# Optimization experiments

Hardware: AMD Instinct MI355X
Metric: run time of the kernel (lower is better)

The kernel has to match this reference:

```python
import jax, jax.numpy as jnp
from jax import lax
import numpy as np

B, N_VARS, M_CLAUSES, K_DIM = 1024, 64, 256, 12
MAX_ITER = 12


def setup_inputs() -> dict:
    key = jax.random.key(0)
    k1, k2, k3, k4 = jax.random.split(key, 4)
    z = jax.random.uniform(k1, (B, N_VARS), dtype=jnp.float32)          # input probabilities
    S = jax.random.normal(k2, (M_CLAUSES, N_VARS + 1), dtype=jnp.float32) * 0.2  # learnable clause matrix (col 0 = truth var)
    w = jax.random.uniform(k3, (M_CLAUSES,), dtype=jnp.float32)          # learnable clause weights
    r = jax.random.normal(k4, (B, N_VARS, K_DIM), dtype=jnp.float32)     # random init directions
    return {"z": z, "S": S, "w": w, "r": r, "max_iter": MAX_ITER}


def _mixing(z, S, w, r, max_iter):
    Bsz, n = z.shape
    m, N = S.shape  # N = n + 1 (truth variable is column 0)
    k = r.shape[-1]
    eps = jnp.float32(1e-8)

    # truth direction v_T = e_0
    vT = jnp.zeros((k,), dtype=z.dtype).at[0].set(1.0)

    # random unit directions orthogonal to v_T (zero out component along e_0)
    r_perp = r.at[..., 0].set(0.0)
    r_perp = r_perp / jnp.maximum(jnp.linalg.norm(r_perp, axis=-1, keepdims=True), eps)

    # SATNet init: v_i = -cos(pi z_i) v_T + sin(pi z_i) r_perp_i
    ang = jnp.pi * z
    Vvars = -jnp.cos(ang)[..., None] * vT + jnp.sin(ang)[..., None] * r_perp  # [B,n,k]
    V = jnp.concatenate([jnp.broadcast_to(vT, (Bsz, 1, k)), Vvars], axis=1)   # [B,N,k]

    Sw = S * w[:, None]                       # weighted clause matrix [m,N]
    W = jnp.einsum('mn,bnk->bmk', Sw, V)      # running product Sw @ V, [B,m,k]
    snrm = jnp.sum(Sw * Sw, axis=0)           # ||s_i||^2 per variable, [N]

    def coord_step(carry, i):
        V, W = carry
        s_i = Sw[:, i]                         # [m]
        v_old = V[:, i, :]                     # [B,k]
        g = jnp.einsum('bmk,m->bk', W, s_i) - snrm[i] * v_old
        v_new = -g / jnp.maximum(jnp.linalg.norm(g, axis=-1, keepdims=True), eps)
        W = W + (v_new - v_old)[:, None, :] * s_i[None, :, None]  # rank-1 update
        V = V.at[:, i, :].set(v_new)
        return (V, W), None

    def sweep(carry, _):
        carry, _ = lax.scan(coord_step, carry, jnp.arange(1, N))  # coordinate descent over variables
        return carry, None

    (V, _), _ = lax.scan(sweep, (V, W), None, length=max_iter)

    # output probabilities: z_i = arccos(-v_i . v_T) / pi
    cos = jnp.clip(-V[:, 1:, 0], -1.0 + 1e-6, 1.0 - 1e-6)
    return jnp.arccos(cos) / jnp.pi


def reference(z, S, w, r, max_iter):
    return _mixing(z, S, w, r, max_iter)
```

## Files before the change

kernel.cpp:

```cpp
#include <hip/hip_runtime.h>
#include <math.h>

#define BATCH 1024
#define NV    64
#define MC    256
#define KD    12
#define PI_F  3.14159265358979323846f

#define CBUF   4544
#define C0OFF  4352
#define DGAOFF 4416
#define DGBOFF 4480

typedef float f2 __attribute__((ext_vector_type(2)));

template <int CTRL>
__device__ __forceinline__ float dpp_addf(float x) {
  int y = __builtin_amdgcn_update_dpp(0, __float_as_int(x), CTRL, 0xF, 0xF, true);
  return x + __int_as_float(y);
}
__device__ __forceinline__ float allreduce16(float x) {
  x = dpp_addf<0xB1>(x);
  x = dpp_addf<0x4E>(x);
  x = dpp_addf<0x124>(x);
  x = dpp_addf<0x128>(x);
  return x;
}
__device__ __forceinline__ float readlane63(float x) {
  return __int_as_float(__builtin_amdgcn_readlane(__float_as_int(x), 63));
}

__global__ void compute_C_kernel(const float* __restrict__ S,
                                 const float* __restrict__ w,
                                 float* __restrict__ Cg, int nsplit) {
  const int q = blockIdx.x;
  const int mc = blockIdx.y;
  const int j = threadIdx.x;
  if (j > NV) return;
  const int v = (q + 1) % 64 + 1;
  const int mlen = MC / nsplit;
  const int m0 = mc * mlen;
  float a0 = 0.f, a1 = 0.f, a2 = 0.f, a3 = 0.f;
  for (int m = m0; m < m0 + mlen; m += 4) {
    const float w0 = w[m], w1 = w[m + 1], w2 = w[m + 2], w3 = w[m + 3];
    a0 = fmaf(S[(m + 0) * (NV + 1) + v] * w0 * w0, S[(m + 0) * (NV + 1) + j], a0);
    a1 = fmaf(S[(m + 1) * (NV + 1) + v] * w1 * w1, S[(m + 1) * (NV + 1) + j], a1);
    a2 = fmaf(S[(m + 2) * (NV + 1) + v] * w2 * w2, S[(m + 2) * (NV + 1) + j], a2);
    a3 = fmaf(S[(m + 3) * (NV + 1) + v] * w3 * w3, S[(m + 3) * (NV + 1) + j], a3);
  }
  const float acc = (a0 + a1) + (a2 + a3);
  float* buf = Cg + mc * CBUF;
  const int p1 = (v == 1) ? 64 : (v - 1);
  const int p2 = (v == 1) ? 63 : (v == 2) ? 64 : (v - 2);
  if (j == 0) buf[C0OFF + q] = acc;
  if (j == p1) buf[DGAOFF + (v - 1)] = acc;
  if (j == p2) buf[DGBOFF + (v - 1)] = acc;
  if (j > 0) {
    const float st = (j == v || j == p1 || j == p2) ? 0.f : acc;
    buf[q * 68 + (j - 1)] = st;
  }
}

__global__ __launch_bounds__(256, 1) void mixing_kernel(
    const float* __restrict__ z, const float* __restrict__ r,
    const float* __restrict__ Cg, const int* __restrict__ max_iter_p,
    float* __restrict__ out, int nsplit) {
  __shared__ float Ls[CBUF];

  const int t = threadIdx.x;
  const int l = t & 63;
  const int kq = l >> 4;
  const int n16 = l & 15;
  const int b = blockIdx.x * 4 + (t >> 6);
  const int max_iter = max_iter_p[0];

  {
    const float4* src = (const float4*)Cg;
    float4* dst = (float4*)Ls;
    for (int idx = t; idx < CBUF / 4; idx += 256) {
      float4 a = src[idx];
      for (int u = 1; u < nsplit; ++u) {
        const float4 p = src[u * (CBUF / 4) + idx];
        a.x += p.x; a.y += p.y; a.z += p.z; a.w += p.w;
      }
      dst[idx] = a;
    }
  }

  const float row0 = (kq == 0) ? 1.f : 0.f;

  f2 V01[4];
  float V2[4];
  #pragma unroll
  for (int s = 0; s < 4; ++s) {
    const int n = 4 * n16 + s;
    const float zv = z[b * NV + n];
    float rp[3];
    float ssp = 0.f;
    #pragma unroll
    for (int j = 0; j < 3; ++j) {
      const int k = 3 * kq + j;
      rp[j] = (k == 0) ? 0.f : r[(b * NV + n) * KD + k];
      ssp = fmaf(rp[j], rp[j], ssp);
    }
    ssp += __shfl_xor(ssp, 16, 64);
    ssp += __shfl_xor(ssp, 32, 64);
    const float inv = 1.f / fmaxf(sqrtf(ssp), 1e-8f);
    float sn, cs;
    sincosf(PI_F * zv, &sn, &cs);
    float vv[3];
    #pragma unroll
    for (int j = 0; j < 3; ++j) {
      const int k = 3 * kq + j;
      vv[j] = (k == 0) ? -cs : sn * rp[j] * inv;
    }
    V01[s].x = vv[0];
    V01[s].y = vv[1];
    V2[s] = vv[2];
  }

  __syncthreads();

  const float4* C4   = (const float4*)Ls;
  const float4* C04  = (const float4*)(Ls + C0OFF);
  const float4* DgA4 = (const float4*)(Ls + DGAOFF);
  const float4* DgB4 = (const float4*)(Ls + DGBOFF);

  f2 P01, vp1_01, vp2_01;
  float P2, vp1_2, vp2_2;

  {
    const float4 ce = C4[63 * 17 + n16];
    const float c0 = Ls[C0OFF + 63];
    f2 q01 = ce.x * V01[0];
    float q2 = ce.x * V2[0];
    q01 = __builtin_elementwise_fma((f2){ce.y, ce.y}, V01[1], q01);
    q2 = fmaf(ce.y, V2[1], q2);
    q01 = __builtin_elementwise_fma((f2){ce.z, ce.z}, V01[2], q01);
    q2 = fmaf(ce.z, V2[2], q2);
    q01 = __builtin_elementwise_fma((f2){ce.w, ce.w}, V01[3], q01);
    q2 = fmaf(ce.w, V2[3], q2);
    q01.x = allreduce16(q01.x);
    q01.y = allreduce16(q01.y);
    q2 = allreduce16(q2);
    q01.x = fmaf(row0, c0, q01.x);
    P01 = q01; P2 = q2;
    const int src = l | 15;
    vp1_01.x = __shfl(V01[3].x, src, 64);
    vp1_01.y = __shfl(V01[3].y, src, 64);
    vp1_2    = __shfl(V2[3],    src, 64);
    vp2_01.x = __shfl(V01[2].x, src, 64);
    vp2_01.y = __shfl(V01[2].y, src, 64);
    vp2_2    = __shfl(V2[2],    src, 64);
  }

  float4 cbA[4], cbB[4], c0A, c0B, daA, daB, dbA, dbB;

  auto prefetch = [&](float4 cb[4], float4& c0b, float4& dab, float4& dbb, int g) {
    #pragma unroll
    for (int s = 0; s < 4; ++s) cb[s] = C4[(4 * g + s) * 17 + n16];
    c0b = C04[g];
    dab = DgA4[g];
    dbb = DgB4[g];
  };

  auto do_group = [&](int ii, const float4 cb[4], const float4& c0b,
                      const float4& dab, const float4& dbb) {
    const bool own  = (n16 == ii);
    const bool ownP = (n16 == ((ii + 15) & 15));
    const float* c0p = &c0b.x;
    const float* dap = &dab.x;
    const float* dbp = &dbb.x;
    #pragma unroll
    for (int s = 0; s < 4; ++s) {
      const float4 ce = cb[s];
      const float db = dbp[s], da = dap[s];

      f2 g01 = __builtin_elementwise_fma((f2){db, db}, vp2_01, P01);
      float g2 = fmaf(db, vp2_2, P2);
      g01 = __builtin_elementwise_fma((f2){da, da}, vp1_01, g01);
      g2 = fmaf(da, vp1_2, g2);

      f2 q01 = ce.x * V01[0];
      float q2 = ce.x * V2[0];
      q01 = __builtin_elementwise_fma((f2){ce.y, ce.y}, V01[1], q01);
      q2 = fmaf(ce.y, V2[1], q2);
      q01 = __builtin_elementwise_fma((f2){ce.z, ce.z}, V01[2], q01);
      q2 = fmaf(ce.z, V2[2], q2);
      q01 = __builtin_elementwise_fma((f2){ce.w, ce.w}, V01[3], q01);
      q2 = fmaf(ce.w, V2[3], q2);

      float n2p = g01.x * g01.x;
      n2p = fmaf(g01.y, g01.y, n2p);
      n2p = fmaf(g2, g2, n2p);

      n2p = dpp_addf<0x142>(n2p);
      q01.x = dpp_addf<0xB1>(q01.x);
      q01.y = dpp_addf<0xB1>(q01.y);
      q2 = dpp_addf<0xB1>(q2);
      n2p = dpp_addf<0x143>(n2p);
      q01.x = dpp_addf<0x4E>(q01.x);
      q01.y = dpp_addf<0x4E>(q01.y);
      q2 = dpp_addf<0x4E>(q2);
      const float n2 = readlane63(n2p);
      q01.x = dpp_addf<0x124>(q01.x);
      q01.y = dpp_addf<0x124>(q01.y);
      q2 = dpp_addf<0x124>(q2);
      const float inv = __builtin_amdgcn_rsqf(fmaxf(n2, 1e-16f));
      q01.x = dpp_addf<0x128>(q01.x);
      q01.y = dpp_addf<0x128>(q01.y);
      q2 = dpp_addf<0x128>(q2);
      const f2 vn01 = g01 * (f2){-inv, -inv};
      const float vn2 = -g2 * inv;
      q01.x = fmaf(row0, c0p[s], q01.x);

      if (s == 0) {
        V01[3].x = ownP ? vp1_01.x : V01[3].x;
        V01[3].y = ownP ? vp1_01.y : V01[3].y;
        V2[3]    = ownP ? vp1_2    : V2[3];
      } else {
        V01[s - 1].x = own ? vp1_01.x : V01[s - 1].x;
        V01[s - 1].y = own ? vp1_01.y : V01[s - 1].y;
        V2[s - 1]    = own ? vp1_2    : V2[s - 1];
      }

      vp2_01 = vp1_01; vp2_2 = vp1_2;
      vp1_01 = vn01;   vp1_2 = vn2;
      P01 = q01;       P2 = q2;
    }
  };

  prefetch(cbA, c0A, daA, dbA, 0);

  for (int it = 0; it < max_iter; ++it) {
    for (int ih = 0; ih < 8; ++ih) {
      prefetch(cbB, c0B, daB, dbB, 2 * ih + 1);
      do_group(2 * ih, cbA, c0A, daA, dbA);
      prefetch(cbA, c0A, daA, dbA, (2 * ih + 2) & 15);
      do_group(2 * ih + 1, cbB, c0B, daB, dbB);
    }
  }

  {
    const bool l15 = (n16 == 15);
    V01[3].x = l15 ? vp1_01.x : V01[3].x;
    V01[3].y = l15 ? vp1_01.y : V01[3].y;
    V2[3]    = l15 ? vp1_2    : V2[3];
  }

  if (kq == 0) {
    float4 o;
    float* op = &o.x;
    #pragma unroll
    for (int s = 0; s < 4; ++s) {
      float cv = -V01[s].x;
      cv = fminf(fmaxf(cv, -1.f + 1e-6f), 1.f - 1e-6f);
      op[s] = acosf(cv) * (1.f / PI_F);
    }
    ((float4*)(out + b * NV))[n16] = o;
  }
}

extern "C" void kernel_launch(void* const* d_in, const int* in_sizes, int n_in,
                              void* d_out, int out_size, void* d_ws, size_t ws_size,
                              hipStream_t stream) {
  const float* z = (const float*)d_in[0];
  const float* S = (const float*)d_in[1];
  const float* w = (const float*)d_in[2];
  const float* r = (const float*)d_in[3];
  const int* max_iter = (const int*)d_in[4];
  float* Cg = (float*)d_ws;

  const int nsplit = (ws_size >= (size_t)8 * CBUF * 4) ? 8
                   : (ws_size >= (size_t)4 * CBUF * 4) ? 4 : 1;
  compute_C_kernel<<<dim3(NV, nsplit), 128, 0, stream>>>(S, w, Cg, nsplit);
  mixing_kernel<<<BATCH / 4, 256, 0, stream>>>(z, r, Cg, max_iter,
                                               (float*)d_out, nsplit);
}
```

Baseline: 147.7 us.

## Compute Gram-matrix products with split-fp16 MFMA and a five-step delayed-update tail

Reworks the coordinate-descent inner loop so the products of the variable-variable coupling matrix with V are computed by 16x16x16 fp16 MFMA instructions. Each operand is split into high and low halves (three MFMAs per chunk) to keep close to fp32 accuracy. Computing four rows per MFMA batch means the last five updated variables must be patched in with scalar diagonal terms, so the layout changes to one lane per k-dimension with readlane broadcasts. This trades the dependent per-variable DPP reduction chain for matrix-core throughput, at the cost of extra MFMA work, an LDS fp16 repack and possible precision loss.

```diff
diff --git a/kernel.cpp b/kernel.cpp
--- a/kernel.cpp
+++ b/kernel.cpp
@@ -1,5 +1,7 @@
 #include <hip/hip_runtime.h>
+#include <hip/hip_fp16.h>
 #include <math.h>
+
 
 #define BATCH 1024
 #define NV    64
@@ -7,12 +9,13 @@
 #define KD    12
 #define PI_F  3.14159265358979323846f
 
-#define CBUF   4544
-#define C0OFF  4352
-#define DGAOFF 4416
-#define DGBOFF 4480
-
-typedef float f2 __attribute__((ext_vector_type(2)));
+#define C0OFF 4352
+#define DGOFF 4416
+#define CBUF  4736
+
+typedef float v4f __attribute__((ext_vector_type(4)));
+typedef _Float16 v4h __attribute__((ext_vector_type(4)));
+typedef unsigned int u2v __attribute__((ext_vector_type(2)));
 
 template <int CTRL>
 __device__ __forceinline__ float dpp_addf(float x) {
@@ -26,18 +29,18 @@
   x = dpp_addf<0x128>(x);
   return x;
 }
-__device__ __forceinline__ float readlane63(float x) {
-  return __int_as_float(__builtin_amdgcn_readlane(__float_as_int(x), 63));
+__device__ __forceinline__ float rlane(float x, int lane) {
+  return __int_as_float(__builtin_amdgcn_readlane(__float_as_int(x), lane));
 }
 
 __global__ void compute_C_kernel(const float* __restrict__ S,
                                  const float* __restrict__ w,
                                  float* __restrict__ Cg, int nsplit) {
-  const int q = blockIdx.x;
+  const int i = blockIdx.x;
   const int mc = blockIdx.y;
   const int j = threadIdx.x;
   if (j > NV) return;
-  const int v = (q + 1) % 64 + 1;
+  const int v = i + 1;
   const int mlen = MC / nsplit;
   const int m0 = mc * mlen;
   float a0 = 0.f, a1 = 0.f, a2 = 0.f, a3 = 0.f;
@@ -50,14 +53,13 @@
   }
   const float acc = (a0 + a1) + (a2 + a3);
   float* buf = Cg + mc * CBUF;
-  const int p1 = (v == 1) ? 64 : (v - 1);
-  const int p2 = (v == 1) ? 63 : (v == 2) ? 64 : (v - 2);
-  if (j == 0) buf[C0OFF + q] = acc;
-  if (j == p1) buf[DGAOFF + (v - 1)] = acc;
-  if (j == p2) buf[DGBOFF + (v - 1)] = acc;
-  if (j > 0) {
-    const float st = (j == v || j == p1 || j == p2) ? 0.f : acc;
-    buf[q * 68 + (j - 1)] = st;
+  if (j == 0) {
+    buf[C0OFF + i] = acc;
+  } else {
+    const int jj = j - 1;
+    const int du = (i - jj + 64) & 63;
+    if (du >= 1 && du <= 5) buf[DGOFF + (du - 1) * 64 + i] = acc;
+    buf[i * 68 + jj] = (du <= 5) ? 0.f : acc;
   }
 }
 
@@ -65,18 +67,19 @@
     const float* __restrict__ z, const float* __restrict__ r,
     const float* __restrict__ Cg, const int* __restrict__ max_iter_p,
     float* __restrict__ out, int nsplit) {
-  __shared__ float Ls[CBUF];
+  __shared__ __align__(16) float Lc[CBUF];
+  __shared__ __align__(16) unsigned short La[8192];
 
   const int t = threadIdx.x;
   const int l = t & 63;
-  const int kq = l >> 4;
-  const int n16 = l & 15;
+  const int n = l & 15;
+  const int lg = l >> 4;
   const int b = blockIdx.x * 4 + (t >> 6);
   const int max_iter = max_iter_p[0];
 
   {
     const float4* src = (const float4*)Cg;
-    float4* dst = (float4*)Ls;
+    float4* dst = (float4*)Lc;
     for (int idx = t; idx < CBUF / 4; idx += 256) {
       float4 a = src[idx];
       for (int u = 1; u < nsplit; ++u) {
@@ -87,177 +90,162 @@
     }
   }
 
-  const float row0 = (kq == 0) ? 1.f : 0.f;
-
-  f2 V01[4];
-  float V2[4];
+  unsigned int Vh[4][2], Vl[4][2];
   #pragma unroll
-  for (int s = 0; s < 4; ++s) {
-    const int n = 4 * n16 + s;
-    const float zv = z[b * NV + n];
-    float rp[3];
-    float ssp = 0.f;
-    #pragma unroll
-    for (int j = 0; j < 3; ++j) {
-      const int k = 3 * kq + j;
-      rp[j] = (k == 0) ? 0.f : r[(b * NV + n) * KD + k];
-      ssp = fmaf(rp[j], rp[j], ssp);
-    }
-    ssp += __shfl_xor(ssp, 16, 64);
-    ssp += __shfl_xor(ssp, 32, 64);
+  for (int c = 0; c < 4; ++c) {
+    #pragma unroll
+    for (int ep = 0; ep < 2; ++ep) {
+      unsigned int hh = 0, ll = 0;
+      #pragma unroll
+      for (int eh = 0; eh < 2; ++eh) {
+        const int var = 16 * c + 4 * lg + 2 * ep + eh;
+        const float zv = z[b * NV + var];
+        float rp = 0.f;
+        if (n >= 1 && n < KD) rp = r[(b * NV + var) * KD + n];
+        const float ssp = allreduce16(rp * rp);
+        const float inv = 1.f / fmaxf(sqrtf(ssp), 1e-8f);
+        const float sn = __builtin_amdgcn_sinf(0.5f * zv);
+        const float cs = __builtin_amdgcn_cosf(0.5f * zv);
+        const float vv = (n == 0) ? -cs : sn * rp * inv;
+        const unsigned int h16 = __half_as_ushort(__float2half(vv));
+        const float hf = __half2float(__ushort_as_half((unsigned short)h16));
+        const unsigned int l16 = __half_as_ushort(__float2half(vv - hf));
+        hh |= h16 << (16 * eh);
+        ll |= l16 << (16 * eh);
+      }
+      Vh[c][ep] = hh;
+      Vl[c][ep] = ll;
+    }
+  }
+  float sh[4];
+  #pragma unroll
+  for (int p = 0; p < 4; ++p) {
+    const float zv = z[b * NV + 16 * p + n];
+    sh[p] = -__builtin_amdgcn_cosf(0.5f * zv);
+  }
+  float vp[6];
+  vp[0] = (n == 0) ? 1.f : 0.f;
+  #pragma unroll
+  for (int u = 1; u <= 5; ++u) {
+    const int var = NV - u;
+    const float zv = z[b * NV + var];
+    float rp = 0.f;
+    if (n >= 1 && n < KD) rp = r[(b * NV + var) * KD + n];
+    const float ssp = allreduce16(rp * rp);
     const float inv = 1.f / fmaxf(sqrtf(ssp), 1e-8f);
-    float sn, cs;
-    sincosf(PI_F * zv, &sn, &cs);
-    float vv[3];
-    #pragma unroll
-    for (int j = 0; j < 3; ++j) {
-      const int k = 3 * kq + j;
-      vv[j] = (k == 0) ? -cs : sn * rp[j] * inv;
-    }
-    V01[s].x = vv[0];
-    V01[s].y = vv[1];
-    V2[s] = vv[2];
+    const float sn = __builtin_amdgcn_sinf(0.5f * zv);
+    const float cs = __builtin_amdgcn_cosf(0.5f * zv);
+    vp[u] = (n == 0) ? -cs : sn * rp * inv;
   }
 
   __syncthreads();
 
-  const float4* C4   = (const float4*)Ls;
-  const float4* C04  = (const float4*)(Ls + C0OFF);
-  const float4* DgA4 = (const float4*)(Ls + DGAOFF);
-  const float4* DgB4 = (const float4*)(Ls + DGBOFF);
-
-  f2 P01, vp1_01, vp2_01;
-  float P2, vp1_2, vp2_2;
-
+  for (int e16 = 0; e16 < 16; ++e16) {
+    const int idx = e16 * 256 + t;
+    const int ri = idx >> 6, jj = idx & 63;
+    const float f = Lc[ri * 68 + jj];
+    const __half h = __float2half(f);
+    const float hf = __half2float(h);
+    const __half lo = __float2half(f - hf);
+    const int G = ri >> 2, m = ri & 3, c = jj >> 4, jc = jj & 15;
+    const int off = ((G * 4 + c) * 2) * 64 + m * 16 + (jc >> 2) * 4 + (jc & 3);
+    La[off] = __half_as_ushort(h);
+    La[off + 64] = __half_as_ushort(lo);
+  }
+  const float t0v = Lc[C0OFF + l];
+  const float t1v = Lc[DGOFF + 0 * 64 + l];
+  const float t2v = Lc[DGOFF + 1 * 64 + l];
+  const float t3v = Lc[DGOFF + 2 * 64 + l];
+  const float t4v = Lc[DGOFF + 3 * 64 + l];
+  const float t5v = Lc[DGOFF + 4 * 64 + l];
+
+  __syncthreads();
+
+  const int aoff = (l & 3) * 16 + lg * 4;
+
+  u2v AH[4], AL[4];
+  auto LOADA = [&](int Gn) {
+    #pragma unroll
+    for (int c = 0; c < 4; ++c) {
+      const int blk = ((Gn * 4 + c) * 2) * 64;
+      AH[c] = *(const u2v*)(&La[blk + aoff]);
+      AL[c] = *(const u2v*)(&La[blk + 64 + aoff]);
+    }
+  };
+  auto MF = [&](u2v a, unsigned int b0, unsigned int b1, v4f acc) -> v4f {
+    u2v bv; bv.x = b0; bv.y = b1;
+    return __builtin_amdgcn_mfma_f32_16x16x16f16(
+        __builtin_bit_cast(v4h, a), __builtin_bit_cast(v4h, bv), acc, 0, 0, 0);
+  };
+  auto MFMA12 = [&](v4f acc) -> v4f {
+    #pragma unroll
+    for (int c = 0; c < 4; ++c) {
+      acc = MF(AH[c], Vh[c][0], Vh[c][1], acc);
+      acc = MF(AH[c], Vl[c][0], Vl[c][1], acc);
+      acc = MF(AL[c], Vh[c][0], Vh[c][1], acc);
+    }
+    return acc;
+  };
+
+  auto TAIL = [&](int i, float q) {
+    const float d0 = rlane(t0v, i), d1 = rlane(t1v, i), d2 = rlane(t2v, i);
+    const float d3 = rlane(t3v, i), d4 = rlane(t4v, i), d5 = rlane(t5v, i);
+    float ga = fmaf(d1, vp[1], fmaf(d0, vp[0], q));
+    float gb = fmaf(d3, vp[3], d2 * vp[2]);
+    float gc = fmaf(d5, vp[5], d4 * vp[4]);
+    const float g = ga + (gb + gc);
+    float n2 = allreduce16(g * g);
+    const float inv = __builtin_amdgcn_rsqf(fmaxf(n2, 1e-16f));
+    const float vn = -g * inv;
+    const float v0 = rlane(vn, 0);
+    {
+      const int pg = i >> 4, ip = i & 15;
+      sh[pg] = (n == ip) ? v0 : sh[pg];
+    }
+    const unsigned int h16 = (unsigned int)__half_as_ushort(__float2half(vn));
+    const float hf = __half2float(__ushort_as_half((unsigned short)h16));
+    const unsigned int l16 = (unsigned int)__half_as_ushort(__float2half(vn - hf));
+    const int c = i >> 4, iv = i & 15;
+    const bool own = (lg == (iv >> 2));
+    const int e = iv & 3, rr = e >> 1, slt = e & 1;
+    const unsigned int oh = Vh[c][rr], ol = Vl[c][rr];
+    const unsigned int nh = slt ? ((oh & 0x0000FFFFu) | (h16 << 16))
+                                : ((oh & 0xFFFF0000u) | h16);
+    const unsigned int nl = slt ? ((ol & 0x0000FFFFu) | (l16 << 16))
+                                : ((ol & 0xFFFF0000u) | l16);
+    Vh[c][rr] = own ? nh : oh;
+    Vl[c][rr] = own ? nl : ol;
+    vp[5] = vp[4]; vp[4] = vp[3]; vp[3] = vp[2]; vp[2] = vp[1]; vp[1] = vn;
+  };
+
+  v4f D;
   {
-    const float4 ce = C4[63 * 17 + n16];
-    const float c0 = Ls[C0OFF + 63];
-    f2 q01 = ce.x * V01[0];
-    float q2 = ce.x * V2[0];
-    q01 = __builtin_elementwise_fma((f2){ce.y, ce.y}, V01[1], q01);
-    q2 = fmaf(ce.y, V2[1], q2);
-    q01 = __builtin_elementwise_fma((f2){ce.z, ce.z}, V01[2], q01);
-    q2 = fmaf(ce.z, V2[2], q2);
-    q01 = __builtin_elementwise_fma((f2){ce.w, ce.w}, V01[3], q01);
-    q2 = fmaf(ce.w, V2[3], q2);
-    q01.x = allreduce16(q01.x);
-    q01.y = allreduce16(q01.y);
-    q2 = allreduce16(q2);
-    q01.x = fmaf(row0, c0, q01.x);
-    P01 = q01; P2 = q2;
-    const int src = l | 15;
-    vp1_01.x = __shfl(V01[3].x, src, 64);
-    vp1_01.y = __shfl(V01[3].y, src, 64);
-    vp1_2    = __shfl(V2[3],    src, 64);
-    vp2_01.x = __shfl(V01[2].x, src, 64);
-    vp2_01.y = __shfl(V01[2].y, src, 64);
-    vp2_2    = __shfl(V2[2],    src, 64);
-  }
-
-  float4 cbA[4], cbB[4], c0A, c0B, daA, daB, dbA, dbB;
-
-  auto prefetch = [&](float4 cb[4], float4& c0b, float4& dab, float4& dbb, int g) {
-    #pragma unroll
-    for (int s = 0; s < 4; ++s) cb[s] = C4[(4 * g + s) * 17 + n16];
-    c0b = C04[g];
-    dab = DgA4[g];
-    dbb = DgB4[g];
-  };
-
-  auto do_group = [&](int ii, const float4 cb[4], const float4& c0b,
-                      const float4& dab, const float4& dbb) {
-    const bool own  = (n16 == ii);
-    const bool ownP = (n16 == ((ii + 15) & 15));
-    const float* c0p = &c0b.x;
-    const float* dap = &dab.x;
-    const float* dbp = &dbb.x;
-    #pragma unroll
-    for (int s = 0; s < 4; ++s) {
-      const float4 ce = cb[s];
-      const float db = dbp[s], da = dap[s];
-
-      f2 g01 = __builtin_elementwise_fma((f2){db, db}, vp2_01, P01);
-      float g2 = fmaf(db, vp2_2, P2);
-      g01 = __builtin_elementwise_fma((f2){da, da}, vp1_01, g01);
-      g2 = fmaf(da, vp1_2, g2);
-
-      f2 q01 = ce.x * V01[0];
-      float q2 = ce.x * V2[0];
-      q01 = __builtin_elementwise_fma((f2){ce.y, ce.y}, V01[1], q01);
-      q2 = fmaf(ce.y, V2[1], q2);
-      q01 = __builtin_elementwise_fma((f2){ce.z, ce.z}, V01[2], q01);
-      q2 = fmaf(ce.z, V2[2], q2);
-      q01 = __builtin_elementwise_fma((f2){ce.w, ce.w}, V01[3], q01);
-      q2 = fmaf(ce.w, V2[3], q2);
-
-      float n2p = g01.x * g01.x;
-      n2p = fmaf(g01.y, g01.y, n2p);
-      n2p = fmaf(g2, g2, n2p);
-
-      n2p = dpp_addf<0x142>(n2p);
-      q01.x = dpp_addf<0xB1>(q01.x);
-      q01.y = dpp_addf<0xB1>(q01.y);
-      q2 = dpp_addf<0xB1>(q2);
-      n2p = dpp_addf<0x143>(n2p);
-      q01.x = dpp_addf<0x4E>(q01.x);
-      q01.y = dpp_addf<0x4E>(q01.y);
-      q2 = dpp_addf<0x4E>(q2);
-      const float n2 = readlane63(n2p);
-      q01.x = dpp_addf<0x124>(q01.x);
-      q01.y = dpp_addf<0x124>(q01.y);
-      q2 = dpp_addf<0x124>(q2);
-      const float inv = __builtin_amdgcn_rsqf(fmaxf(n2, 1e-16f));
-      q01.x = dpp_addf<0x128>(q01.x);
-      q01.y = dpp_addf<0x128>(q01.y);
-      q2 = dpp_addf<0x128>(q2);
-      const f2 vn01 = g01 * (f2){-inv, -inv};
-      const float vn2 = -g2 * inv;
-      q01.x = fmaf(row0, c0p[s], q01.x);
-
-      if (s == 0) {
-        V01[3].x = ownP ? vp1_01.x : V01[3].x;
-        V01[3].y = ownP ? vp1_01.y : V01[3].y;
-        V2[3]    = ownP ? vp1_2    : V2[3];
-      } else {
-        V01[s - 1].x = own ? vp1_01.x : V01[s - 1].x;
-        V01[s - 1].y = own ? vp1_01.y : V01[s - 1].y;
-        V2[s - 1]    = own ? vp1_2    : V2[s - 1];
-      }
-
-      vp2_01 = vp1_01; vp2_2 = vp1_2;
-      vp1_01 = vn01;   vp1_2 = vn2;
-      P01 = q01;       P2 = q2;
-    }
-  };
-
-  prefetch(cbA, c0A, daA, dbA, 0);
+    v4f zz = {0.f, 0.f, 0.f, 0.f};
+    LOADA(0);
+    D = MFMA12(zz);
+  }
 
   for (int it = 0; it < max_iter; ++it) {
-    for (int ih = 0; ih < 8; ++ih) {
-      prefetch(cbB, c0B, daB, dbB, 2 * ih + 1);
-      do_group(2 * ih, cbA, c0A, daA, dbA);
-      prefetch(cbA, c0A, daA, dbA, (2 * ih + 2) & 15);
-      do_group(2 * ih + 1, cbB, c0B, daB, dbB);
-    }
-  }
-
-  {
-    const bool l15 = (n16 == 15);
-    V01[3].x = l15 ? vp1_01.x : V01[3].x;
-    V01[3].y = l15 ? vp1_01.y : V01[3].y;
-    V2[3]    = l15 ? vp1_2    : V2[3];
-  }
-
-  if (kq == 0) {
-    float4 o;
-    float* op = &o.x;
-    #pragma unroll
-    for (int s = 0; s < 4; ++s) {
-      float cv = -V01[s].x;
+    #pragma unroll
+    for (int G = 0; G < 16; ++G) {
+      LOADA((G + 1) & 15);
+      TAIL(4 * G + 0, D[0]);
+      TAIL(4 * G + 1, D[1]);
+      v4f zz = {0.f, 0.f, 0.f, 0.f};
+      v4f Dn = MFMA12(zz);
+      TAIL(4 * G + 2, D[2]);
+      TAIL(4 * G + 3, D[3]);
+      D = Dn;
+    }
+  }
+
+  if (l < 16) {
+    #pragma unroll
+    for (int p = 0; p < 4; ++p) {
+      float cv = -sh[p];
       cv = fminf(fmaxf(cv, -1.f + 1e-6f), 1.f - 1e-6f);
-      op[s] = acosf(cv) * (1.f / PI_F);
-    }
-    ((float4*)(out + b * NV))[n16] = o;
+      out[b * NV + 16 * p + l] = acosf(cv) * (1.f / PI_F);
+    }
   }
 }
 
```

New measurement: 162.5 us. 10.0% more time.
